# Kernel tuning notes

Hardware: AMD Instinct MI355X
Metric: run time of the kernel (lower is better)

Reference implementation:

```python
import jax, jax.numpy as jnp
import numpy as np

B, S, E, H = 4, 2048, 1024, 16
D = E // H  # head_dim = 64

def setup_inputs() -> dict:
    key = jax.random.key(0)
    k1, k2, k3 = jax.random.split(key, 3)
    x = jax.random.normal(k1, (B, S, E), dtype=jnp.float32)
    # Linear weights stored as [in, out] so y = x @ W (torch Linear uses W^T; same math).
    w_att = jax.random.normal(k2, (E, 3 * E), dtype=jnp.float32) * (1.0 / np.sqrt(E))
    w_proj = jax.random.normal(k3, (E, E), dtype=jnp.float32) * (1.0 / np.sqrt(E))
    return {"x": x, "w_att": w_att, "w_proj": w_proj}

def reference(x, w_att, w_proj):
    b, s, e = x.shape
    qkv = x @ w_att                      # [b, s, 3e]
    q, k, v = jnp.split(qkv, 3, axis=-1)
    # [b, h, s, d]
    q = q.reshape(b, s, H, D).transpose(0, 2, 1, 3)
    k = k.reshape(b, s, H, D).transpose(0, 2, 1, 3)
    v = v.reshape(b, s, H, D).transpose(0, 2, 1, 3)
    scale = 1.0 / np.sqrt(D)
    att = jnp.einsum('bhqd,bhkd->bhqk', q, k) * scale  # [b, h, s, s]
    causal = jnp.tril(jnp.ones((s, s), dtype=bool))
    att = jnp.where(causal[None, None], att, jnp.finfo(att.dtype).min)
    att = jax.nn.softmax(att, axis=-1)
    y = jnp.einsum('bhqk,bhkd->bhqd', att, v)          # [b, h, s, d]
    y = y.transpose(0, 2, 1, 3).reshape(b, s, e)
    return y @ w_proj
```

## Files before the change

### kernel.cpp

```cpp
#include <hip/hip_runtime.h>
#include <hip/hip_bf16.h>

typedef __bf16 b16v8 __attribute__((ext_vector_type(8)));
typedef __bf16 b16v4 __attribute__((ext_vector_type(4)));
typedef float  f32x4 __attribute__((ext_vector_type(4)));

#define BB 4
#define SS 2048
#define EE 1024
#define HH 16
#define DD 64

#define QSCALE 0.18033688011112042f

__device__ __forceinline__ void async16(const __bf16* g, __bf16* l) {
  typedef __attribute__((address_space(1))) const unsigned int gu32;
  typedef __attribute__((address_space(3))) unsigned int lu32;
  __builtin_amdgcn_global_load_lds((gu32*)g, (lu32*)l, 16, 0, 0);
}

__device__ __forceinline__ f32x4 mfma16x16x16_bf16(b16v4 a, b16v4 b, f32x4 c) {
#if __has_builtin(__builtin_amdgcn_mfma_f32_16x16x16_bf16)
  return __builtin_amdgcn_mfma_f32_16x16x16_bf16(a, b, c, 0, 0, 0);
#else
  typedef short s16v4 __attribute__((ext_vector_type(4)));
  union U { b16v4 h; s16v4 s; };
  U ua, ub; ua.h = a; ub.h = b;
  return __builtin_amdgcn_mfma_f32_16x16x16bf16_1k(ua.s, ub.s, c, 0, 0, 0);
#endif
}

__global__ __launch_bounds__(256) void cast_x_kernel(const float* __restrict__ in,
                                                     __bf16* __restrict__ out, int n4) {
  int i = blockIdx.x * 256 + threadIdx.x;
  if (i >= n4) return;
  float4 f = ((const float4*)in)[i];
  b16v4 o = {(__bf16)f.x, (__bf16)f.y, (__bf16)f.z, (__bf16)f.w};
  ((b16v4*)out)[i] = o;
}

__global__ __launch_bounds__(256) void cast_transpose(const float* __restrict__ w,
                                                      __bf16* __restrict__ wt, int K, int N) {
  __shared__ float t[32][33];
  int n0 = blockIdx.x * 32, k0 = blockIdx.y * 32;
  int tx = threadIdx.x & 31, ty = threadIdx.x >> 5;
#pragma unroll
  for (int j = 0; j < 32; j += 8)
    t[ty + j][tx] = w[(size_t)(k0 + ty + j) * N + n0 + tx];
  __syncthreads();
#pragma unroll
  for (int j = 0; j < 32; j += 8)
    wt[(size_t)(n0 + ty + j) * K + k0 + tx] = (__bf16)t[tx][ty + j];
}

template <int EPI>
__global__ __launch_bounds__(256) void gemm_bt(const __bf16* __restrict__ A,
                                               const __bf16* __restrict__ Bt,
                                               void* C0, void* C1, void* C2,
                                               int M, int N, int K) {
  __shared__ __bf16 a_lds[2][128 * 32];
  __shared__ __bf16 b_lds[2][128 * 32];
  const int tid = threadIdx.x;
  const int lane = tid & 63;
  const int w = tid >> 6;
  const int wm = (w >> 1) * 64, wn = (w & 1) * 64;
  const int l16 = lane & 15, quad = lane >> 4;
  const __bf16* Ab = A + (size_t)blockIdx.y * 128 * K;
  const __bf16* Bb = Bt + (size_t)blockIdx.x * 128 * K;

  auto stage = [&](int k0, int bufi) {
#pragma unroll
    for (int i = 0; i < 2; ++i) {
      int c = tid + i * 256;
      int row = c >> 2, ch = c & 3;
      async16(Ab + (size_t)row * K + k0 + ((ch ^ (row & 3)) * 8), a_lds[bufi] + c * 8);
    }
#pragma unroll
    for (int i = 0; i < 2; ++i) {
      int c = tid + i * 256;
      int row = c >> 2, ch = c & 3;
      async16(Bb + (size_t)row * K + k0 + ((ch ^ (row & 3)) * 8), b_lds[bufi] + c * 8);
    }
  };

  f32x4 acc[4][4];
#pragma unroll
  for (int i = 0; i < 4; ++i)
#pragma unroll
    for (int j = 0; j < 4; ++j) acc[i][j] = f32x4{0.f, 0.f, 0.f, 0.f};

  stage(0, 0);
  const int KT = K >> 5;
  const int sw = (quad ^ (l16 & 3)) * 8;
  for (int kt = 0; kt < KT; ++kt) {
    __syncthreads();
    if (kt + 1 < KT) stage((kt + 1) << 5, (kt + 1) & 1);
    const __bf16* ab = a_lds[kt & 1];
    const __bf16* bb = b_lds[kt & 1];
    b16v8 af[4], bf4[4];
#pragma unroll
    for (int t = 0; t < 4; ++t) {
      af[t] = *(const b16v8*)(ab + (wm + t * 16 + l16) * 32 + sw);
      bf4[t] = *(const b16v8*)(bb + (wn + t * 16 + l16) * 32 + sw);
    }
#pragma unroll
    for (int mt = 0; mt < 4; ++mt)
#pragma unroll
      for (int nt = 0; nt < 4; ++nt)
        acc[mt][nt] = __builtin_amdgcn_mfma_f32_16x16x32_bf16(af[mt], bf4[nt], acc[mt][nt], 0, 0, 0);
  }

  if (EPI == 0) {
    __bf16* qb = (__bf16*)C0;
    __bf16* kb = (__bf16*)C1;
    __bf16* vtb = (__bf16*)C2;
#pragma unroll
    for (int mt = 0; mt < 4; ++mt)
#pragma unroll
      for (int nt = 0; nt < 4; ++nt) {
        int row = blockIdx.y * 128 + wm + mt * 16 + quad * 4;
        int col = blockIdx.x * 128 + wn + nt * 16 + l16;
        int b = row >> 11, s = row & 2047;
        int sec = col >> 10, cc = col & 1023;
        int h = cc >> 6, d = cc & 63;
        if (sec == 2) {
          b16v4 vv = {(__bf16)acc[mt][nt][0], (__bf16)acc[mt][nt][1],
                      (__bf16)acc[mt][nt][2], (__bf16)acc[mt][nt][3]};
          *(b16v4*)(vtb + ((size_t)(b * HH + h) * DD + d) * SS + s) = vv;
        } else {
          __bf16* dst = (sec == 0) ? qb : kb;
          float sc = (sec == 0) ? QSCALE : 1.0f;
#pragma unroll
          for (int r = 0; r < 4; ++r)
            dst[(((size_t)(b * HH + h) * SS + s + r) << 6) + d] = (__bf16)(acc[mt][nt][r] * sc);
        }
      }
  } else {
    float* out = (float*)C0;
#pragma unroll
    for (int mt = 0; mt < 4; ++mt)
#pragma unroll
      for (int nt = 0; nt < 4; ++nt)
#pragma unroll
        for (int r = 0; r < 4; ++r) {
          int row = blockIdx.y * 128 + wm + mt * 16 + quad * 4 + r;
          int col = blockIdx.x * 128 + wn + nt * 16 + l16;
          out[(size_t)row * N + col] = acc[mt][nt][r];
        }
  }
}

__global__ __launch_bounds__(256, 2) void attn_kernel(const __bf16* __restrict__ qb,
                                                      const __bf16* __restrict__ kb,
                                                      const __bf16* __restrict__ vtb,
                                                      __bf16* __restrict__ y) {
  __shared__ __bf16 kv_lds[2][16384];
  const int tid = threadIdx.x;
  const int lane = tid & 63;
  const int w = tid >> 6;
  const int l16 = lane & 15, quad = lane >> 4;
  const int p = blockIdx.x, bh = blockIdx.y;
  const int b = bh >> 4, h = bh & 15;
  const __bf16* kbase = kb + (size_t)bh * SS * DD;
  const __bf16* vtbase = vtb + (size_t)bh * DD * SS;

  auto stage = [&](int j, __bf16* buf) {
#pragma unroll
    for (int i = 0; i < 4; ++i) {
      int L = w * 256 + i * 64 + lane;
      int row = L >> 3, c = L & 7;
      async16(kbase + (size_t)(j * 128 + row) * DD + ((c ^ (row & 7)) * 8), buf + L * 8);
    }
#pragma unroll
    for (int i = 0; i < 4; ++i) {
      int L = w * 256 + i * 64 + lane;
      int d = L >> 4, c = L & 15;
      async16(vtbase + (size_t)d * SS + j * 128 + ((c ^ (d & 15)) * 8), buf + 8192 + L * 8);
    }
  };

#pragma unroll
  for (int t = 0; t < 2; ++t) {
    const int qt = (t == 0) ? (15 - p) : p;

    b16v8 qf[2][2];
#pragma unroll
    for (int qtile = 0; qtile < 2; ++qtile)
#pragma unroll
      for (int ks = 0; ks < 2; ++ks)
        qf[qtile][ks] = *(const b16v8*)(qb + ((size_t)bh * SS + qt * 128 + w * 32 + qtile * 16 + l16) * DD + ks * 32 + quad * 8);

    f32x4 o[4][2];
#pragma unroll
    for (int dt = 0; dt < 4; ++dt)
#pragma unroll
      for (int qtile = 0; qtile < 2; ++qtile) o[dt][qtile] = f32x4{0.f, 0.f, 0.f, 0.f};
    float mrow[2] = {-1e30f, -1e30f}, lrow[2] = {0.f, 0.f};

    __syncthreads();
    stage(0, kv_lds[0]);

    for (int j = 0; j <= qt; ++j) {
      __syncthreads();
      if (j < qt) stage(j + 1, kv_lds[(j + 1) & 1]);
      const __bf16* kbuf = kv_lds[j & 1];
      const __bf16* vbuf = kbuf + 8192;

      f32x4 s[2][8];
#pragma unroll
      for (int qtile = 0; qtile < 2; ++qtile)
#pragma unroll
        for (int kf = 0; kf < 8; ++kf) s[qtile][kf] = f32x4{0.f, 0.f, 0.f, 0.f};
#pragma unroll
      for (int kf = 0; kf < 8; ++kf) {
        int rb = kf * 16 + l16;
        b16v8 kf0 = *(const b16v8*)(kbuf + rb * DD + ((quad ^ (rb & 7)) * 8));
        b16v8 kf1 = *(const b16v8*)(kbuf + rb * DD + (((quad + 4) ^ (rb & 7)) * 8));
#pragma unroll
        for (int qtile = 0; qtile < 2; ++qtile) {
          s[qtile][kf] = __builtin_amdgcn_mfma_f32_16x16x32_bf16(kf0, qf[qtile][0], s[qtile][kf], 0, 0, 0);
          s[qtile][kf] = __builtin_amdgcn_mfma_f32_16x16x32_bf16(kf1, qf[qtile][1], s[qtile][kf], 0, 0, 0);
        }
      }
      if (j == qt) {
#pragma unroll
        for (int qtile = 0; qtile < 2; ++qtile) {
          int ql = w * 32 + qtile * 16 + l16;
#pragma unroll
          for (int kf = 0; kf < 8; ++kf)
#pragma unroll
            for (int r = 0; r < 4; ++r)
              if (kf * 16 + quad * 4 + r > ql) s[qtile][kf][r] = -1e30f;
        }
      }
#pragma unroll
      for (int qtile = 0; qtile < 2; ++qtile) {
        float mx = s[qtile][0][0];
#pragma unroll
        for (int kf = 0; kf < 8; ++kf)
#pragma unroll
          for (int r = 0; r < 4; ++r) mx = fmaxf(mx, s[qtile][kf][r]);
        mx = fmaxf(mx, __shfl_xor(mx, 16));
        mx = fmaxf(mx, __shfl_xor(mx, 32));
        float mn = fmaxf(mrow[qtile], mx);
        float alpha = __builtin_amdgcn_exp2f(mrow[qtile] - mn);
        mrow[qtile] = mn;
        float rs = 0.f;
#pragma unroll
        for (int kf = 0; kf < 8; ++kf)
#pragma unroll
          for (int r = 0; r < 4; ++r) {
            float pv = __builtin_amdgcn_exp2f(s[qtile][kf][r] - mn);
            s[qtile][kf][r] = pv;
            rs += pv;
          }
        rs += __shfl_xor(rs, 16);
        rs += __shfl_xor(rs, 32);
        lrow[qtile] = lrow[qtile] * alpha + rs;
#pragma unroll
        for (int dt = 0; dt < 4; ++dt)
#pragma unroll
          for (int r = 0; r < 4; ++r) o[dt][qtile][r] *= alpha;
      }
#pragma unroll
      for (int kf = 0; kf < 8; ++kf) {
        b16v4 pf[2];
#pragma unroll
        for (int qtile = 0; qtile < 2; ++qtile) {
          b16v4 pk = {(__bf16)s[qtile][kf][0], (__bf16)s[qtile][kf][1],
                      (__bf16)s[qtile][kf][2], (__bf16)s[qtile][kf][3]};
          pf[qtile] = pk;
        }
        int cg = kf * 2 + (quad >> 1);
#pragma unroll
        for (int dt = 0; dt < 4; ++dt) {
          int d = dt * 16 + l16;
          b16v4 vf = *(const b16v4*)(vbuf + d * 128 + ((cg ^ l16) * 8) + ((quad & 1) * 4));
#pragma unroll
          for (int qtile = 0; qtile < 2; ++qtile)
            o[dt][qtile] = mfma16x16x16_bf16(vf, pf[qtile], o[dt][qtile]);
        }
      }
    }

#pragma unroll
    for (int qtile = 0; qtile < 2; ++qtile) {
      float inv = 1.0f / lrow[qtile];
      int q = qt * 128 + w * 32 + qtile * 16 + l16;
#pragma unroll
      for (int dt = 0; dt < 4; ++dt) {
        b16v4 ov = {(__bf16)(o[dt][qtile][0] * inv), (__bf16)(o[dt][qtile][1] * inv),
                    (__bf16)(o[dt][qtile][2] * inv), (__bf16)(o[dt][qtile][3] * inv)};
        *(b16v4*)(y + ((size_t)b * SS + q) * EE + h * 64 + dt * 16 + quad * 4) = ov;
      }
    }
  }
}

extern "C" void kernel_launch(void* const* d_in, const int* in_sizes, int n_in,
                              void* d_out, int out_size, void* d_ws, size_t ws_size,
                              hipStream_t stream) {
  (void)in_sizes; (void)n_in; (void)out_size; (void)ws_size;
  const float* x = (const float*)d_in[0];
  const float* w_att = (const float*)d_in[1];
  const float* w_proj = (const float*)d_in[2];
  float* out = (float*)d_out;

  char* ws = (char*)d_ws;
  size_t off = 0;
  auto alloc = [&](size_t elems) { __bf16* p = (__bf16*)(ws + off); off += elems * 2; return p; };
  __bf16* xb = alloc(8388608);
  __bf16* qb = alloc(8388608);
  __bf16* kb = alloc(8388608);
  __bf16* vtb = alloc(8388608);
  __bf16* watt = alloc(3145728);
  __bf16* wproj = alloc(1048576);

  cast_x_kernel<<<8192, 256, 0, stream>>>(x, xb, 2097152);
  cast_transpose<<<dim3(96, 32), 256, 0, stream>>>(w_att, watt, 1024, 3072);
  cast_transpose<<<dim3(32, 32), 256, 0, stream>>>(w_proj, wproj, 1024, 1024);
  gemm_bt<0><<<dim3(24, 64), 256, 0, stream>>>(xb, watt, qb, kb, vtb, 8192, 3072, 1024);
  attn_kernel<<<dim3(8, 64), 256, 0, stream>>>(qb, kb, vtb, xb);
  gemm_bt<1><<<dim3(8, 64), 256, 0, stream>>>(xb, wproj, out, nullptr, nullptr, 8192, 1024, 1024);
}
```

Before: 256.6 us.

## Halve attention tile to 64 queries and 64 keys, raise occupancy

```diff
diff --git a/kernel.cpp b/kernel.cpp
--- a/kernel.cpp
+++ b/kernel.cpp
@@ -150,52 +150,48 @@
   }
 }
 
-__global__ __launch_bounds__(256, 2) void attn_kernel(const __bf16* __restrict__ qb,
+__global__ __launch_bounds__(256, 4) void attn_kernel(const __bf16* __restrict__ qb,
                                                       const __bf16* __restrict__ kb,
                                                       const __bf16* __restrict__ vtb,
                                                       __bf16* __restrict__ y) {
-  __shared__ __bf16 kv_lds[2][16384];
+  __shared__ __bf16 kv_lds[2][8192];
   const int tid = threadIdx.x;
   const int lane = tid & 63;
   const int w = tid >> 6;
   const int l16 = lane & 15, quad = lane >> 4;
-  const int p = blockIdx.x, bh = blockIdx.y;
+  const int bh = blockIdx.x, p = blockIdx.y;
   const int b = bh >> 4, h = bh & 15;
   const __bf16* kbase = kb + (size_t)bh * SS * DD;
   const __bf16* vtbase = vtb + (size_t)bh * DD * SS;
 
   auto stage = [&](int j, __bf16* buf) {
 #pragma unroll
-    for (int i = 0; i < 4; ++i) {
-      int L = w * 256 + i * 64 + lane;
+    for (int i = 0; i < 2; ++i) {
+      int L = tid + i * 256;
       int row = L >> 3, c = L & 7;
-      async16(kbase + (size_t)(j * 128 + row) * DD + ((c ^ (row & 7)) * 8), buf + L * 8);
-    }
-#pragma unroll
-    for (int i = 0; i < 4; ++i) {
-      int L = w * 256 + i * 64 + lane;
-      int d = L >> 4, c = L & 15;
-      async16(vtbase + (size_t)d * SS + j * 128 + ((c ^ (d & 15)) * 8), buf + 8192 + L * 8);
+      async16(kbase + (size_t)(j * 64 + row) * DD + ((c ^ (row & 7)) * 8), buf + L * 8);
+    }
+#pragma unroll
+    for (int i = 0; i < 2; ++i) {
+      int L = tid + i * 256;
+      int d = L >> 3, c = L & 7;
+      async16(vtbase + (size_t)d * SS + j * 64 + ((c ^ (d & 7)) * 8), buf + 4096 + L * 8);
     }
   };
 
 #pragma unroll
   for (int t = 0; t < 2; ++t) {
-    const int qt = (t == 0) ? (15 - p) : p;
-
-    b16v8 qf[2][2];
-#pragma unroll
-    for (int qtile = 0; qtile < 2; ++qtile)
-#pragma unroll
-      for (int ks = 0; ks < 2; ++ks)
-        qf[qtile][ks] = *(const b16v8*)(qb + ((size_t)bh * SS + qt * 128 + w * 32 + qtile * 16 + l16) * DD + ks * 32 + quad * 8);
-
-    f32x4 o[4][2];
-#pragma unroll
-    for (int dt = 0; dt < 4; ++dt)
-#pragma unroll
-      for (int qtile = 0; qtile < 2; ++qtile) o[dt][qtile] = f32x4{0.f, 0.f, 0.f, 0.f};
-    float mrow[2] = {-1e30f, -1e30f}, lrow[2] = {0.f, 0.f};
+    const int qt = (t == 0) ? (31 - p) : p;
+
+    b16v8 qf[2];
+#pragma unroll
+    for (int ks = 0; ks < 2; ++ks)
+      qf[ks] = *(const b16v8*)(qb + ((size_t)bh * SS + qt * 64 + w * 16 + l16) * DD + ks * 32 + quad * 8);
+
+    f32x4 o[4];
+#pragma unroll
+    for (int dt = 0; dt < 4; ++dt) o[dt] = f32x4{0.f, 0.f, 0.f, 0.f};
+    float mrow = -1e30f, lrow = 0.f;
 
     __syncthreads();
     stage(0, kv_lds[0]);
@@ -204,95 +200,73 @@
       __syncthreads();
       if (j < qt) stage(j + 1, kv_lds[(j + 1) & 1]);
       const __bf16* kbuf = kv_lds[j & 1];
-      const __bf16* vbuf = kbuf + 8192;
-
-      f32x4 s[2][8];
-#pragma unroll
-      for (int qtile = 0; qtile < 2; ++qtile)
-#pragma unroll
-        for (int kf = 0; kf < 8; ++kf) s[qtile][kf] = f32x4{0.f, 0.f, 0.f, 0.f};
-#pragma unroll
-      for (int kf = 0; kf < 8; ++kf) {
+      const __bf16* vbuf = kbuf + 4096;
+
+      f32x4 s[4];
+#pragma unroll
+      for (int kf = 0; kf < 4; ++kf) s[kf] = f32x4{0.f, 0.f, 0.f, 0.f};
+#pragma unroll
+      for (int kf = 0; kf < 4; ++kf) {
         int rb = kf * 16 + l16;
         b16v8 kf0 = *(const b16v8*)(kbuf + rb * DD + ((quad ^ (rb & 7)) * 8));
         b16v8 kf1 = *(const b16v8*)(kbuf + rb * DD + (((quad + 4) ^ (rb & 7)) * 8));
-#pragma unroll
-        for (int qtile = 0; qtile < 2; ++qtile) {
-          s[qtile][kf] = __builtin_amdgcn_mfma_f32_16x16x32_bf16(kf0, qf[qtile][0], s[qtile][kf], 0, 0, 0);
-          s[qtile][kf] = __builtin_amdgcn_mfma_f32_16x16x32_bf16(kf1, qf[qtile][1], s[qtile][kf], 0, 0, 0);
-        }
+        s[kf] = __builtin_amdgcn_mfma_f32_16x16x32_bf16(kf0, qf[0], s[kf], 0, 0, 0);
+        s[kf] = __builtin_amdgcn_mfma_f32_16x16x32_bf16(kf1, qf[1], s[kf], 0, 0, 0);
       }
       if (j == qt) {
-#pragma unroll
-        for (int qtile = 0; qtile < 2; ++qtile) {
-          int ql = w * 32 + qtile * 16 + l16;
-#pragma unroll
-          for (int kf = 0; kf < 8; ++kf)
-#pragma unroll
-            for (int r = 0; r < 4; ++r)
-              if (kf * 16 + quad * 4 + r > ql) s[qtile][kf][r] = -1e30f;
-        }
-      }
-#pragma unroll
-      for (int qtile = 0; qtile < 2; ++qtile) {
-        float mx = s[qtile][0][0];
-#pragma unroll
-        for (int kf = 0; kf < 8; ++kf)
-#pragma unroll
-          for (int r = 0; r < 4; ++r) mx = fmaxf(mx, s[qtile][kf][r]);
-        mx = fmaxf(mx, __shfl_xor(mx, 16));
-        mx = fmaxf(mx, __shfl_xor(mx, 32));
-        float mn = fmaxf(mrow[qtile], mx);
-        float alpha = __builtin_amdgcn_exp2f(mrow[qtile] - mn);
-        mrow[qtile] = mn;
-        float rs = 0.f;
-#pragma unroll
-        for (int kf = 0; kf < 8; ++kf)
-#pragma unroll
-          for (int r = 0; r < 4; ++r) {
-            float pv = __builtin_amdgcn_exp2f(s[qtile][kf][r] - mn);
-            s[qtile][kf][r] = pv;
-            rs += pv;
-          }
-        rs += __shfl_xor(rs, 16);
-        rs += __shfl_xor(rs, 32);
-        lrow[qtile] = lrow[qtile] * alpha + rs;
-#pragma unroll
-        for (int dt = 0; dt < 4; ++dt)
-#pragma unroll
-          for (int r = 0; r < 4; ++r) o[dt][qtile][r] *= alpha;
-      }
-#pragma unroll
-      for (int kf = 0; kf < 8; ++kf) {
-        b16v4 pf[2];
-#pragma unroll
-        for (int qtile = 0; qtile < 2; ++qtile) {
-          b16v4 pk = {(__bf16)s[qtile][kf][0], (__bf16)s[qtile][kf][1],
-                      (__bf16)s[qtile][kf][2], (__bf16)s[qtile][kf][3]};
-          pf[qtile] = pk;
-        }
+        int ql = w * 16 + l16;
+#pragma unroll
+        for (int kf = 0; kf < 4; ++kf)
+#pragma unroll
+          for (int r = 0; r < 4; ++r)
+            if (kf * 16 + quad * 4 + r > ql) s[kf][r] = -1e30f;
+      }
+      float mx = s[0][0];
+#pragma unroll
+      for (int kf = 0; kf < 4; ++kf)
+#pragma unroll
+        for (int r = 0; r < 4; ++r) mx = fmaxf(mx, s[kf][r]);
+      mx = fmaxf(mx, __shfl_xor(mx, 16));
+      mx = fmaxf(mx, __shfl_xor(mx, 32));
+      float mn = fmaxf(mrow, mx);
+      float alpha = __builtin_amdgcn_exp2f(mrow - mn);
+      mrow = mn;
+      float rs = 0.f;
+#pragma unroll
+      for (int kf = 0; kf < 4; ++kf)
+#pragma unroll
+        for (int r = 0; r < 4; ++r) {
+          float pv = __builtin_amdgcn_exp2f(s[kf][r] - mn);
+          s[kf][r] = pv;
+          rs += pv;
+        }
+      rs += __shfl_xor(rs, 16);
+      rs += __shfl_xor(rs, 32);
+      lrow = lrow * alpha + rs;
+#pragma unroll
+      for (int dt = 0; dt < 4; ++dt)
+#pragma unroll
+        for (int r = 0; r < 4; ++r) o[dt][r] *= alpha;
+#pragma unroll
+      for (int kf = 0; kf < 4; ++kf) {
+        b16v4 pf = {(__bf16)s[kf][0], (__bf16)s[kf][1], (__bf16)s[kf][2], (__bf16)s[kf][3]};
         int cg = kf * 2 + (quad >> 1);
 #pragma unroll
         for (int dt = 0; dt < 4; ++dt) {
           int d = dt * 16 + l16;
-          b16v4 vf = *(const b16v4*)(vbuf + d * 128 + ((cg ^ l16) * 8) + ((quad & 1) * 4));
-#pragma unroll
-          for (int qtile = 0; qtile < 2; ++qtile)
-            o[dt][qtile] = mfma16x16x16_bf16(vf, pf[qtile], o[dt][qtile]);
-        }
-      }
-    }
-
-#pragma unroll
-    for (int qtile = 0; qtile < 2; ++qtile) {
-      float inv = 1.0f / lrow[qtile];
-      int q = qt * 128 + w * 32 + qtile * 16 + l16;
-#pragma unroll
-      for (int dt = 0; dt < 4; ++dt) {
-        b16v4 ov = {(__bf16)(o[dt][qtile][0] * inv), (__bf16)(o[dt][qtile][1] * inv),
-                    (__bf16)(o[dt][qtile][2] * inv), (__bf16)(o[dt][qtile][3] * inv)};
-        *(b16v4*)(y + ((size_t)b * SS + q) * EE + h * 64 + dt * 16 + quad * 4) = ov;
-      }
+          b16v4 vf = *(const b16v4*)(vbuf + d * 64 + ((cg ^ (d & 7)) * 8) + ((quad & 1) * 4));
+          o[dt] = mfma16x16x16_bf16(vf, pf, o[dt]);
+        }
+      }
+    }
+
+    float inv = 1.0f / lrow;
+    int q = qt * 64 + w * 16 + l16;
+#pragma unroll
+    for (int dt = 0; dt < 4; ++dt) {
+      b16v4 ov = {(__bf16)(o[dt][0] * inv), (__bf16)(o[dt][1] * inv),
+                  (__bf16)(o[dt][2] * inv), (__bf16)(o[dt][3] * inv)};
+      *(b16v4*)(y + ((size_t)b * SS + q) * EE + h * 64 + dt * 16 + quad * 4) = ov;
     }
   }
 }
@@ -320,6 +294,6 @@
   cast_transpose<<<dim3(96, 32), 256, 0, stream>>>(w_att, watt, 1024, 3072);
   cast_transpose<<<dim3(32, 32), 256, 0, stream>>>(w_proj, wproj, 1024, 1024);
   gemm_bt<0><<<dim3(24, 64), 256, 0, stream>>>(xb, watt, qb, kb, vtb, 8192, 3072, 1024);
-  attn_kernel<<<dim3(8, 64), 256, 0, stream>>>(qb, kb, vtb, xb);
+  attn_kernel<<<dim3(64, 16), 256, 0, stream>>>(qb, kb, vtb, xb);
   gemm_bt<1><<<dim3(8, 64), 256, 0, stream>>>(xb, wproj, out, nullptr, nullptr, 8192, 1024, 1024);
 }
```

Result: slower. 264.4 us (+3.0%).
